# Kernel tuning notes

Measured on AMD Instinct MI355X. Metric: run time of the kernel, lower is better.

Reference implementation:

```python
import jax, jax.numpy as jnp
from jax import lax
import numpy as np

NF, G, K = 64, 8, 3
B, H, W = 4, 128, 128
KK = K * K
CG = NF // G  # channels per deformable group


def setup_inputs() -> dict:
    key = jax.random.key(0)
    ks = jax.random.split(key, 8)
    f32 = jnp.float32
    s = 0.05  # small init so predicted offsets stay in a realistic range
    return {
        'nbr_fea_l': jax.random.normal(ks[0], (B, NF, H, W), f32),
        'ref_fea_l': jax.random.normal(ks[1], (B, NF, H, W), f32),
        'w_off1': jax.random.normal(ks[2], (NF, 2 * NF, K, K), f32) * s,
        'b_off1': jax.random.normal(ks[3], (NF,), f32) * s,
        'w_om': jax.random.normal(ks[4], (3 * G * KK, NF, K, K), f32) * s,
        'b_om': jax.random.normal(ks[5], (3 * G * KK,), f32) * s,
        'w_dcn': jax.random.normal(ks[6], (NF, NF, K, K), f32) * s,
        'b_dcn': jax.random.normal(ks[7], (NF,), f32) * s,
    }


def _conv3(x, w, b):
    # 3x3, stride 1, pad 1, NCHW/OIHW
    y = lax.conv_general_dilated(x, w, (1, 1), ((1, 1), (1, 1)))
    return y + b[None, :, None, None]


def _lrelu(x):
    return jnp.where(x >= 0, x, 0.1 * x)


def _gather_one(xf, idx):
    # xf: [CG, H*W], idx: [KK, H, W] -> [CG, KK, H, W]
    return jnp.take(xf, idx, axis=1)


_gather = jax.vmap(jax.vmap(_gather_one))  # over B, G


def _bilinear(x_flat, py, px):
    # x_flat: [B,G,CG,H*W]; py/px: [B,G,KK,H,W] sample coords
    y0f = jnp.floor(py)
    x0f = jnp.floor(px)
    wy = py - y0f
    wx = px - x0f
    y0 = y0f.astype(jnp.int32)
    x0 = x0f.astype(jnp.int32)
    out = jnp.zeros(x_flat.shape[:3] + py.shape[2:], x_flat.dtype)
    corners = [(0, 0, (1 - wy) * (1 - wx)), (0, 1, (1 - wy) * wx),
               (1, 0, wy * (1 - wx)), (1, 1, wy * wx)]
    for dy, dx, wgt in corners:
        yy = y0 + dy
        xx = x0 + dx
        valid = ((yy >= 0) & (yy < H) & (xx >= 0) & (xx < W)).astype(x_flat.dtype)
        idx = jnp.clip(yy, 0, H - 1) * W + jnp.clip(xx, 0, W - 1)
        g = _gather(x_flat, idx)  # [B,G,CG,KK,H,W]
        out = out + g * (wgt * valid)[:, :, None]
    return out


def _forward(nbr, ref, w_off1, b_off1, w_om, b_om, w_dcn, b_dcn):
    # offset feature branch
    off_feat = _lrelu(_conv3(jnp.concatenate([nbr, ref], axis=1), w_off1, b_off1))
    om = _conv3(off_feat, w_om, b_om)  # [B, 3*G*KK, H, W]
    o1, o2, m = jnp.split(om, 3, axis=1)
    off_y = o1.reshape(B, G, KK, H, W)
    off_x = o2.reshape(B, G, KK, H, W)
    mask = jax.nn.sigmoid(m).reshape(B, G, KK, H, W)
    # kernel tap displacements (pad=1, dilation=1, stride=1)
    dy = (jnp.repeat(jnp.arange(K), K) - 1).astype(nbr.dtype)  # [KK]
    dx = (jnp.tile(jnp.arange(K), K) - 1).astype(nbr.dtype)
    hh = jnp.arange(H, dtype=nbr.dtype)
    ww = jnp.arange(W, dtype=nbr.dtype)
    py = hh[None, None, None, :, None] + dy[None, None, :, None, None] + off_y
    px = ww[None, None, None, None, :] + dx[None, None, :, None, None] + off_x
    x_flat = nbr.reshape(B, G, CG, H * W)
    sampled = _bilinear(x_flat, py, px)           # [B,G,CG,KK,H,W]
    sampled = sampled * mask[:, :, None]          # modulated (DCNv2)
    w = w_dcn.reshape(NF, G, CG, KK)
    out = jnp.einsum('bgckhw,ogck->bohw', sampled, w) + b_dcn[None, :, None, None]
    return _lrelu(out)


def reference(nbr_fea_l, ref_fea_l, w_off1, b_off1, w_om, b_om, w_dcn, b_dcn):
    return _forward(nbr_fea_l, ref_fea_l, w_off1, b_off1, w_om, b_om, w_dcn, b_dcn)
```

## Files before the change

kernel.cpp:

```cpp
#include <hip/hip_runtime.h>
#include <hip/hip_bf16.h>
#include <hip/hip_fp16.h>
#include <cmath>

#define NF 64
#define GRP 8
#define CG 8
#define KK 9
#define HH 128
#define WWID 128
#define BB 4
#define HWSZ (HH * WWID)
#define C_OM 216
#define OMS 292
#define DPS 72

typedef __attribute__((ext_vector_type(8))) short bf16x8;
typedef __attribute__((ext_vector_type(8))) _Float16 f16x8;
typedef __attribute__((ext_vector_type(4))) float f32x4;

__device__ inline unsigned short f2bf(float f) {
    union { float f; unsigned u; } x; x.f = f;
    unsigned r = x.u + 0x7fff + ((x.u >> 16) & 1);
    return (unsigned short)(r >> 16);
}

__global__ __launch_bounds__(256) void prep_kernel(
    const float* __restrict__ nbr, const float* __restrict__ ref,
    const float* __restrict__ w1, const float* __restrict__ wom,
    const float* __restrict__ wdcn,
    unsigned short* __restrict__ out, unsigned short* __restrict__ gm,
    unsigned short* __restrict__ wf1, unsigned short* __restrict__ wf2,
    unsigned short* __restrict__ wdf)
{
    __shared__ unsigned short lds[64 * 136];
    __shared__ __half lds_h[64 * 72];
    const int tid = threadIdx.x;

    if (blockIdx.x < 1024) {
        const int blk = blockIdx.x;
        const int b = blk >> 8, rem = blk & 255, y = rem >> 1, x0 = (rem & 1) * 64;
        const size_t rowoff = (size_t)y * WWID + x0;

        for (int it = 0; it < 32; ++it) {
            int idx = it * 256 + tid;
            int c = idx >> 6, p = idx & 63;
            const float* src = (c < NF) ? (nbr + (size_t)(b * NF + c) * HWSZ)
                                        : (ref + (size_t)(b * NF + c - NF) * HWSZ);
            const float v = src[rowoff + p];
            lds[p * 136 + c] = f2bf(v);
            if (c < 64) lds_h[p * 72 + c] = __float2half(v);
        }
        __syncthreads();
        const int p = tid >> 2, c0 = (tid & 3) * 32;
        unsigned short* dst = out + ((size_t)b * HWSZ + rowoff + p) * 128 + c0;
#pragma unroll
        for (int i = 0; i < 8; ++i)
            *(int2*)(dst + i * 4) = *(const int2*)&lds[p * 136 + c0 + i * 4];
        if (c0 < 64) {
#pragma unroll
            for (int gi = 0; gi < 4; ++gi) {
                const int g = (c0 >> 3) + gi;
                *(int4*)(gm + (((size_t)(b * 8 + g)) * HWSZ + rowoff + p) * 8) =
                    *(const int4*)&lds_h[p * 72 + g * 8];
            }
        }
        return;
    }

    int idx = (blockIdx.x - 1024) * 256 + tid;
    if (idx < 73728) {
        int j = idx & 7, lane = (idx >> 3) & 63, t = idx >> 9;
        int mt = t % 4, kt = t / 4;
        int c0 = (kt / 9) * 32, tap = kt - (kt / 9) * 9;
        int cout = mt * 16 + (lane & 15);
        int cin = c0 + ((lane >> 4) * 8) + j;
        wf1[idx] = f2bf(w1[((size_t)cout * 128 + cin) * KK + tap]);
        return;
    }
    idx -= 73728;
    if (idx < 129024) {
        int j = idx & 7, lane = (idx >> 3) & 63, t = idx >> 9;
        int mt = t % 14, kt = t / 14;
        int c0 = (kt / 9) * 32, tap = kt - (kt / 9) * 9;
        int cout = mt * 16 + (lane & 15);
        int cin = c0 + ((lane >> 4) * 8) + j;
        float v = (cout < C_OM) ? wom[((size_t)cout * 64 + cin) * KK + tap] : 0.f;
        wf2[idx] = f2bf(v);
        return;
    }
    idx -= 129024;
    if (idx < 36864) {
        int j = idx & 7, lane = (idx >> 3) & 63, t = idx >> 9;
        int mt = t & 3, s = t >> 2;
        int cout = mt * 16 + (lane & 15);
        int kglob = s * 32 + (lane >> 4) * 8 + j;
        int gk = kglob >> 3, c = kglob & 7;
        int g = gk / 9, kt = gk - g * 9;
        const __half hv = __float2half(wdcn[((size_t)cout * NF + g * 8 + c) * 9 + kt]);
        wdf[idx] = *(const unsigned short*)&hv;
    }
}

__global__ __launch_bounds__(256) void conv1_kernel(
    const unsigned short* __restrict__ in,
    const unsigned short* __restrict__ wf,
    const float* __restrict__ bias,
    unsigned short* __restrict__ dst)
{
    __shared__ unsigned short st[3 * 66 * DPS];

    const int tid = threadIdx.x;
    const int lane = tid & 63;
    const int wv = tid >> 6;
    const int ng = blockIdx.x;
    const int b = ng >> 8, rem = ng & 255;
    const int y = rem >> 1, x0 = (rem & 1) * 64;
    const int ln = lane & 15, kb = lane >> 4;

    f32x4 acc[4];
#pragma unroll
    for (int nt = 0; nt < 4; ++nt) acc[nt] = f32x4{0.f, 0.f, 0.f, 0.f};

    for (int ch0 = 0; ch0 < 128; ch0 += 64) {
        __syncthreads();
        for (int i = tid; i < 3 * 66 * 8; i += 256) {
            const int j = i & 7, t = i >> 3;
            const int px = t % 66, r = t / 66;
            const int yy = y + r - 1, xx = x0 + px - 1;
            int4 v = {0, 0, 0, 0};
            if ((unsigned)yy < (unsigned)HH && (unsigned)xx < (unsigned)WWID)
                v = *(const int4*)(in + ((size_t)b * HWSZ + yy * WWID + xx) * 128
                                      + ch0 + j * 8);
            *(int4*)&st[(r * 66 + px) * DPS + j * 8] = v;
        }
        __syncthreads();

#pragma unroll
        for (int cc = 0; cc < 64; cc += 32) {
#pragma unroll
            for (int tap = 0; tap < 9; ++tap) {
                const int ky = tap / 3, kx = tap % 3;
                const int kt = ((ch0 + cc) / 32) * 9 + tap;
                const bf16x8 afrag =
                    *(const bf16x8*)(wf + (((size_t)kt * 4 + wv) * 64 + lane) * 8);
                bf16x8 bfrag[4];
#pragma unroll
                for (int nt = 0; nt < 4; ++nt) {
                    const int px = nt * 16 + ln + kx;
                    bfrag[nt] = *(const bf16x8*)&st[(ky * 66 + px) * DPS + cc + kb * 8];
                }
#pragma unroll
                for (int nt = 0; nt < 4; ++nt)
                    acc[nt] = __builtin_amdgcn_mfma_f32_16x16x32_bf16(
                        afrag, bfrag[nt], acc[nt], 0, 0, 0);
            }
        }
    }

    const int cout = wv * 16 + kb * 4;
    const float b0 = bias[cout], b1 = bias[cout + 1];
    const float b2 = bias[cout + 2], b3 = bias[cout + 3];
#pragma unroll
    for (int nt = 0; nt < 4; ++nt) {
        const int px = x0 + nt * 16 + ln;
        const size_t pix = (size_t)b * HWSZ + (size_t)y * WWID + px;
        f32x4 v = acc[nt];
        v[0] += b0; v[1] += b1; v[2] += b2; v[3] += b3;
#pragma unroll
        for (int r = 0; r < 4; ++r) v[r] = (v[r] >= 0.f) ? v[r] : 0.1f * v[r];
        int2 pk;
        pk.x = (int)f2bf(v[0]) | ((int)f2bf(v[1]) << 16);
        pk.y = (int)f2bf(v[2]) | ((int)f2bf(v[3]) << 16);
        *(int2*)(dst + pix * 64 + cout) = pk;
    }
}

__global__ __launch_bounds__(256, 4) void dcn_fused_kernel(
    const unsigned short* __restrict__ off_f,
    const unsigned short* __restrict__ gm,
    const unsigned short* __restrict__ wf2,
    const float* __restrict__ bom,
    const unsigned short* __restrict__ wdf,
    const float* __restrict__ bdcn,
    float* __restrict__ out)
{
    __shared__ unsigned short smem[64 * OMS];

    const int raw = blockIdx.x;
    const int bid = (raw & 7) * 128 + (raw >> 3);
    const int b = bid >> 8;
    const int rem = bid & 255;
    const int y = rem >> 1;
    const int x0 = (rem & 1) * 64;

    const int tid = threadIdx.x;
    const int lane = tid & 63;
    const int wv = tid >> 6;
    const int ln = lane & 15, kb = lane >> 4;

    for (int i = tid; i < 3 * 66 * 8; i += 256) {
        const int j = i & 7, t = i >> 3;
        const int px = t % 66, r = t / 66;
        const int yy = y + r - 1, xx = x0 + px - 1;
        int4 v = {0, 0, 0, 0};
        if ((unsigned)yy < (unsigned)HH && (unsigned)xx < (unsigned)WWID)
            v = *(const int4*)(off_f + ((size_t)b * HWSZ + yy * WWID + xx) * 64 + j * 8);
        *(int4*)&smem[(r * 66 + px) * DPS + j * 8] = v;
    }
    __syncthreads();

    f32x4 acc1[4][4];
#pragma unroll
    for (int i = 0; i < 4; ++i)
#pragma unroll
        for (int j = 0; j < 4; ++j) acc1[i][j] = f32x4{0.f, 0.f, 0.f, 0.f};

    {
        bf16x8 afA[4], afB[4];
#pragma unroll
        for (int i = 0; i < 4; ++i) {
            const int mt = wv + 4 * i;
            afA[i] = (mt < 14)
                ? ((const bf16x8*)wf2)[(size_t)0 * 14 * 64 + (size_t)mt * 64 + lane]
                : bf16x8{};
        }

#pragma unroll
        for (int step = 0; step < 18; ++step) {
            const int cc = (step / 9) * 32;
            const int tap = step % 9;
            const int ky = tap / 3, kx = tap % 3;

            if (step < 17) {
                const int kt1 = step + 1;
                bf16x8* alt = (step & 1) ? afA : afB;
#pragma unroll
                for (int i = 0; i < 4; ++i) {
                    const int mt = wv + 4 * i;
                    alt[i] = (mt < 14)
                        ? ((const bf16x8*)wf2)[(size_t)kt1 * 14 * 64 + (size_t)mt * 64 + lane]
                        : bf16x8{};
                }
            }

            bf16x8 bfrag[4];
#pragma unroll
            for (int nt = 0; nt < 4; ++nt) {
                const int px = nt * 16 + ln + kx;
                bfrag[nt] = *(const bf16x8*)&smem[(ky * 66 + px) * DPS + cc + kb * 8];
            }

            const bf16x8* cur = (step & 1) ? afB : afA;
#pragma unroll
            for (int i = 0; i < 4; ++i) {
                const int mt = wv + 4 * i;
                if (mt < 14) {
#pragma unroll
                    for (int nt = 0; nt < 4; ++nt)
                        acc1[i][nt] = __builtin_amdgcn_mfma_f32_16x16x32_bf16(
                            cur[i], bfrag[nt], acc1[i][nt], 0, 0, 0);
                }
            }
        }
    }
    __syncthreads();

    __half* smh = (__half*)smem;
#pragma unroll
    for (int i = 0; i < 4; ++i) {
        const int mt = wv + 4 * i;
        if (mt >= 14) continue;
        const int cb = mt * 16 + kb * 4;
#pragma unroll
        for (int nt = 0; nt < 4; ++nt) {
            const int px = nt * 16 + ln;
#pragma unroll
            for (int r = 0; r < 4; ++r) {
                const int c = cb + r;
                if (c < C_OM) {
                    const int field = (c >= 144) ? 2 : ((c >= 72) ? 1 : 0);
                    const int gk = c - field * 72;
                    float v = acc1[i][nt][r] + bom[c];
                    if (field == 2) v = 1.f / (1.f + __expf(-v));
                    smh[px * OMS + gk * 4 + field] = __float2half(v);
                }
            }
        }
    }
    __syncthreads();

    const int pxl = wv * 16 + ln;
    const int x = x0 + pxl;

    f32x4 acc[4];
#pragma unroll
    for (int mt = 0; mt < 4; ++mt) acc[mt] = f32x4{0.f, 0.f, 0.f, 0.f};

    const unsigned short* gmb = gm + (size_t)b * 8 * HWSZ * 8;

#pragma unroll
    for (int ch = 0; ch < 3; ++ch) {
        short4 q[6];
#pragma unroll
        for (int i = 0; i < 6; ++i) {
            const int gk = (ch * 6 + i) * 4 + kb;
            q[i] = *(const short4*)&smh[pxl * OMS + gk * 4];
        }

#pragma unroll
        for (int i = 0; i < 6; ++i) {
            const int s = ch * 6 + i;
            const int gk = s * 4 + kb;
            const int g = gk / 9;
            const int kt = gk - g * 9;

            const float oy = __half2float(((const __half*)&q[i])[0]);
            const float ox = __half2float(((const __half*)&q[i])[1]);
            const float mv = __half2float(((const __half*)&q[i])[2]);

            const float pyf = (float)(y + kt / 3 - 1) + oy;
            const float pxf = (float)(x + kt % 3 - 1) + ox;
            const float fy = floorf(pyf), fx = floorf(pxf);
            const float wy = pyf - fy, wx = pxf - fx;
            const int iy = (int)fy, ix = (int)fx;

            float w00 = (1.f - wy) * (1.f - wx);
            float w01 = (1.f - wy) * wx;
            float w10 = wy * (1.f - wx);
            float w11 = wy * wx;

            const bool vy0 = (iy >= 0) && (iy < HH);
            const bool vy1 = (iy + 1 >= 0) && (iy + 1 < HH);
            const bool vx0 = (ix >= 0) && (ix < WWID);
            const bool vx1 = (ix + 1 >= 0) && (ix + 1 < WWID);
            w00 *= (vy0 && vx0) ? mv : 0.f;
            w01 *= (vy0 && vx1) ? mv : 0.f;
            w10 *= (vy1 && vx0) ? mv : 0.f;
            w11 *= (vy1 && vx1) ? mv : 0.f;

            const int y0c = min(max(iy, 0), HH - 1);
            const int y1c = min(max(iy + 1, 0), HH - 1);
            const int x0c = min(max(ix, 0), WWID - 1);
            const int x1c = min(max(ix + 1, 0), WWID - 1);
            const int sel = x1c - x0c;

            const float wl0 = w00 + (sel ? 0.f : w01);
            const float wh0 = sel ? w01 : 0.f;
            const float wl1 = w10 + (sel ? 0.f : w11);
            const float wh1 = sel ? w11 : 0.f;

            const unsigned short* pgm = gmb + (size_t)g * HWSZ * 8;
            const size_t rec0 = (size_t)(y0c * WWID + x0c) * 8;
            const size_t rec1 = (size_t)(y1c * WWID + x0c) * 8;
            int4 L0 = *(const int4*)(pgm + rec0);
            int4 H0 = *(const int4*)(pgm + rec0 + 8);
            int4 L1 = *(const int4*)(pgm + rec1);
            int4 H1 = *(const int4*)(pgm + rec1 + 8);

            const __half2 wl0h = __float2half2_rn(wl0);
            const __half2 wh0h = __float2half2_rn(wh0);
            const __half2 wl1h = __float2half2_rn(wl1);
            const __half2 wh1h = __float2half2_rn(wh1);
            const __half2* l0 = (const __half2*)&L0;
            const __half2* h0 = (const __half2*)&H0;
            const __half2* l1 = (const __half2*)&L1;
            const __half2* h1 = (const __half2*)&H1;
            __half2 bp0 = __hfma2(l0[0], wl0h, __hfma2(h0[0], wh0h,
                          __hfma2(l1[0], wl1h, __hmul2(h1[0], wh1h))));
            __half2 bp1 = __hfma2(l0[1], wl0h, __hfma2(h0[1], wh0h,
                          __hfma2(l1[1], wl1h, __hmul2(h1[1], wh1h))));
            __half2 bp2 = __hfma2(l0[2], wl0h, __hfma2(h0[2], wh0h,
                          __hfma2(l1[2], wl1h, __hmul2(h1[2], wh1h))));
            __half2 bp3 = __hfma2(l0[3], wl0h, __hfma2(h0[3], wh0h,
                          __hfma2(l1[3], wl1h, __hmul2(h1[3], wh1h))));
            __half2 bpv[4] = {bp0, bp1, bp2, bp3};
            const f16x8 bfrag = *(const f16x8*)bpv;

            const f16x8* af = (const f16x8*)wdf + ((size_t)s * 4) * 64 + lane;
#pragma unroll
            for (int mt = 0; mt < 4; ++mt)
                acc[mt] = __builtin_amdgcn_mfma_f32_16x16x32_f16(
                    af[(size_t)mt * 64], bfrag, acc[mt], 0, 0, 0);
        }
    }

#pragma unroll
    for (int mt = 0; mt < 4; ++mt) {
#pragma unroll
        for (int r = 0; r < 4; ++r) {
            const int cout = mt * 16 + kb * 4 + r;
            float v = acc[mt][r] + bdcn[cout];
            v = (v >= 0.f) ? v : 0.1f * v;
            out[((size_t)(b * NF + cout)) * HWSZ + (size_t)y * WWID + x] = v;
        }
    }
}

extern "C" void kernel_launch(void* const* d_in, const int* in_sizes, int n_in,
                              void* d_out, int out_size, void* d_ws, size_t ws_size,
                              hipStream_t stream)
{
    const float* nbr  = (const float*)d_in[0];
    const float* ref  = (const float*)d_in[1];
    const float* w1   = (const float*)d_in[2];
    const float* b1   = (const float*)d_in[3];
    const float* wom  = (const float*)d_in[4];
    const float* bom  = (const float*)d_in[5];
    const float* wdcn = (const float*)d_in[6];
    const float* bdcn = (const float*)d_in[7];
    float* out = (float*)d_out;

    const size_t NH_B  = (size_t)BB * HWSZ * 128 * 2;
    const size_t OFF_B = (size_t)BB * HWSZ * 64 * 2;
    const size_t GM_B  = (size_t)BB * HWSZ * 64 * 2 + 64;
    const size_t WF1_B = 36 * 4 * 512 * 2;
    const size_t WF2_B = 18 * 14 * 512 * 2;

    char* ws = (char*)d_ws;
    unsigned short* nhwcin = (unsigned short*)ws;
    unsigned short* off_f  = (unsigned short*)(ws + NH_B);
    unsigned short* gm     = (unsigned short*)(ws + NH_B + OFF_B);
    unsigned short* wf1    = (unsigned short*)(ws + NH_B + OFF_B + GM_B);
    unsigned short* wf2    = wf1 + WF1_B / 2;
    unsigned short* wdf    = wf2 + WF2_B / 2;

    prep_kernel<<<1024 + 936, 256, 0, stream>>>(
        nbr, ref, w1, wom, wdcn, nhwcin, gm, wf1, wf2, wdf);

    conv1_kernel<<<1024, 256, 0, stream>>>(nhwcin, wf1, b1, off_f);

    dcn_fused_kernel<<<1024, 256, 0, stream>>>(
        off_f, gm, wf2, bom, wdf, bdcn, out);
}
```

Before: 90.01 us.

## Widen DCN tile to full row, vectorize prep loads, double-buffer conv1 weights

The fused DCN kernel now handles a full 128-pixel row per 512-thread block, so the halo of the offset features is loaded once per row and each wave covers 8 pixel tiles with 2 channel tiles. The prep kernel reads inputs as float4 rather than scalars, and conv1 prefetches the next weight fragment while issuing MFMAs on the current one. The larger block doubles LDS use and changes occupancy and register pressure, and the launch-bounds hint of 4 blocks of 512 threads may be unreachable.

Result: no change. 88.38 us (median of 2 runs) (-1.8%).

```diff
diff --git a/kernel.cpp b/kernel.cpp
--- a/kernel.cpp
+++ b/kernel.cpp
@@ -42,14 +42,20 @@
         const int b = blk >> 8, rem = blk & 255, y = rem >> 1, x0 = (rem & 1) * 64;
         const size_t rowoff = (size_t)y * WWID + x0;
 
-        for (int it = 0; it < 32; ++it) {
+#pragma unroll
+        for (int it = 0; it < 8; ++it) {
             int idx = it * 256 + tid;
-            int c = idx >> 6, p = idx & 63;
+            int c = idx >> 4, p4 = idx & 15;
             const float* src = (c < NF) ? (nbr + (size_t)(b * NF + c) * HWSZ)
                                         : (ref + (size_t)(b * NF + c - NF) * HWSZ);
-            const float v = src[rowoff + p];
-            lds[p * 136 + c] = f2bf(v);
-            if (c < 64) lds_h[p * 72 + c] = __float2half(v);
+            const float4 v = *(const float4*)(src + rowoff + p4 * 4);
+            const float vv[4] = {v.x, v.y, v.z, v.w};
+#pragma unroll
+            for (int k = 0; k < 4; ++k) {
+                const int p = p4 * 4 + k;
+                lds[p * 136 + c] = f2bf(vv[k]);
+                if (c < 64) lds_h[p * 72 + c] = __float2half(vv[k]);
+            }
         }
         __syncthreads();
         const int p = tid >> 2, c0 = (tid & 3) * 32;
@@ -136,25 +142,34 @@
         }
         __syncthreads();
 
-#pragma unroll
-        for (int cc = 0; cc < 64; cc += 32) {
-#pragma unroll
-            for (int tap = 0; tap < 9; ++tap) {
-                const int ky = tap / 3, kx = tap % 3;
-                const int kt = ((ch0 + cc) / 32) * 9 + tap;
-                const bf16x8 afrag =
-                    *(const bf16x8*)(wf + (((size_t)kt * 4 + wv) * 64 + lane) * 8);
-                bf16x8 bfrag[4];
-#pragma unroll
-                for (int nt = 0; nt < 4; ++nt) {
-                    const int px = nt * 16 + ln + kx;
-                    bfrag[nt] = *(const bf16x8*)&st[(ky * 66 + px) * DPS + cc + kb * 8];
-                }
-#pragma unroll
-                for (int nt = 0; nt < 4; ++nt)
-                    acc[nt] = __builtin_amdgcn_mfma_f32_16x16x32_bf16(
-                        afrag, bfrag[nt], acc[nt], 0, 0, 0);
-            }
+        const int base_kt = (ch0 / 32) * 9;
+        bf16x8 afA, afB;
+        afA = *(const bf16x8*)(wf + (((size_t)base_kt * 4 + wv) * 64 + lane) * 8);
+
+#pragma unroll
+        for (int step = 0; step < 18; ++step) {
+            const int cc = (step / 9) * 32;
+            const int tap = step % 9;
+            const int ky = tap / 3, kx = tap % 3;
+
+            if (step < 17) {
+                const int kt1 = base_kt + step + 1;
+                bf16x8* alt = (step & 1) ? &afA : &afB;
+                *alt = *(const bf16x8*)(wf + (((size_t)kt1 * 4 + wv) * 64 + lane) * 8);
+            }
+
+            bf16x8 bfrag[4];
+#pragma unroll
+            for (int nt = 0; nt < 4; ++nt) {
+                const int px = nt * 16 + ln + kx;
+                bfrag[nt] = *(const bf16x8*)&st[(ky * 66 + px) * DPS + cc + kb * 8];
+            }
+
+            const bf16x8 cur = (step & 1) ? afB : afA;
+#pragma unroll
+            for (int nt = 0; nt < 4; ++nt)
+                acc[nt] = __builtin_amdgcn_mfma_f32_16x16x32_bf16(
+                    cur, bfrag[nt], acc[nt], 0, 0, 0);
         }
     }
 
@@ -176,7 +191,7 @@
     }
 }
 
-__global__ __launch_bounds__(256, 4) void dcn_fused_kernel(
+__global__ __launch_bounds__(512, 4) void dcn_fused_kernel(
     const unsigned short* __restrict__ off_f,
     const unsigned short* __restrict__ gm,
     const unsigned short* __restrict__ wf2,
@@ -185,44 +200,42 @@
     const float* __restrict__ bdcn,
     float* __restrict__ out)
 {
-    __shared__ unsigned short smem[64 * OMS];
+    __shared__ unsigned short smem[128 * OMS];
 
     const int raw = blockIdx.x;
-    const int bid = (raw & 7) * 128 + (raw >> 3);
-    const int b = bid >> 8;
-    const int rem = bid & 255;
-    const int y = rem >> 1;
-    const int x0 = (rem & 1) * 64;
+    const int bid = (raw & 7) * 64 + (raw >> 3);
+    const int b = bid >> 7;
+    const int y = bid & 127;
 
     const int tid = threadIdx.x;
     const int lane = tid & 63;
     const int wv = tid >> 6;
     const int ln = lane & 15, kb = lane >> 4;
 
-    for (int i = tid; i < 3 * 66 * 8; i += 256) {
+    for (int i = tid; i < 3 * 130 * 8; i += 512) {
         const int j = i & 7, t = i >> 3;
-        const int px = t % 66, r = t / 66;
-        const int yy = y + r - 1, xx = x0 + px - 1;
+        const int px = t % 130, r = t / 130;
+        const int yy = y + r - 1, xx = px - 1;
         int4 v = {0, 0, 0, 0};
         if ((unsigned)yy < (unsigned)HH && (unsigned)xx < (unsigned)WWID)
             v = *(const int4*)(off_f + ((size_t)b * HWSZ + yy * WWID + xx) * 64 + j * 8);
-        *(int4*)&smem[(r * 66 + px) * DPS + j * 8] = v;
+        *(int4*)&smem[(r * 130 + px) * DPS + j * 8] = v;
     }
     __syncthreads();
 
-    f32x4 acc1[4][4];
-#pragma unroll
-    for (int i = 0; i < 4; ++i)
-#pragma unroll
-        for (int j = 0; j < 4; ++j) acc1[i][j] = f32x4{0.f, 0.f, 0.f, 0.f};
+    f32x4 acc1[2][8];
+#pragma unroll
+    for (int i = 0; i < 2; ++i)
+#pragma unroll
+        for (int j = 0; j < 8; ++j) acc1[i][j] = f32x4{0.f, 0.f, 0.f, 0.f};
 
     {
-        bf16x8 afA[4], afB[4];
-#pragma unroll
-        for (int i = 0; i < 4; ++i) {
-            const int mt = wv + 4 * i;
+        bf16x8 afA[2], afB[2];
+#pragma unroll
+        for (int i = 0; i < 2; ++i) {
+            const int mt = wv + 8 * i;
             afA[i] = (mt < 14)
-                ? ((const bf16x8*)wf2)[(size_t)0 * 14 * 64 + (size_t)mt * 64 + lane]
+                ? ((const bf16x8*)wf2)[(size_t)mt * 64 + lane]
                 : bf16x8{};
         }
 
@@ -236,28 +249,28 @@
                 const int kt1 = step + 1;
                 bf16x8* alt = (step & 1) ? afA : afB;
 #pragma unroll
-                for (int i = 0; i < 4; ++i) {
-                    const int mt = wv + 4 * i;
+                for (int i = 0; i < 2; ++i) {
+                    const int mt = wv + 8 * i;
                     alt[i] = (mt < 14)
                         ? ((const bf16x8*)wf2)[(size_t)kt1 * 14 * 64 + (size_t)mt * 64 + lane]
                         : bf16x8{};
                 }
             }
 
-            bf16x8 bfrag[4];
-#pragma unroll
-            for (int nt = 0; nt < 4; ++nt) {
+            bf16x8 bfrag[8];
+#pragma unroll
+            for (int nt = 0; nt < 8; ++nt) {
                 const int px = nt * 16 + ln + kx;
-                bfrag[nt] = *(const bf16x8*)&smem[(ky * 66 + px) * DPS + cc + kb * 8];
+                bfrag[nt] = *(const bf16x8*)&smem[(ky * 130 + px) * DPS + cc + kb * 8];
             }
 
             const bf16x8* cur = (step & 1) ? afB : afA;
 #pragma unroll
-            for (int i = 0; i < 4; ++i) {
-                const int mt = wv + 4 * i;
+            for (int i = 0; i < 2; ++i) {
+                const int mt = wv + 8 * i;
                 if (mt < 14) {
 #pragma unroll
-                    for (int nt = 0; nt < 4; ++nt)
+                    for (int nt = 0; nt < 8; ++nt)
                         acc1[i][nt] = __builtin_amdgcn_mfma_f32_16x16x32_bf16(
                             cur[i], bfrag[nt], acc1[i][nt], 0, 0, 0);
                 }
@@ -268,12 +281,12 @@
 
     __half* smh = (__half*)smem;
 #pragma unroll
-    for (int i = 0; i < 4; ++i) {
-        const int mt = wv + 4 * i;
+    for (int i = 0; i < 2; ++i) {
+        const int mt = wv + 8 * i;
         if (mt >= 14) continue;
         const int cb = mt * 16 + kb * 4;
 #pragma unroll
-        for (int nt = 0; nt < 4; ++nt) {
+        for (int nt = 0; nt < 8; ++nt) {
             const int px = nt * 16 + ln;
 #pragma unroll
             for (int r = 0; r < 4; ++r) {
@@ -291,7 +304,7 @@
     __syncthreads();
 
     const int pxl = wv * 16 + ln;
-    const int x = x0 + pxl;
+    const int x = pxl;
 
     f32x4 acc[4];
 #pragma unroll
@@ -430,6 +443,6 @@
 
     conv1_kernel<<<1024, 256, 0, stream>>>(nhwcin, wf1, b1, off_f);
 
-    dcn_fused_kernel<<<1024, 256, 0, stream>>>(
+    dcn_fused_kernel<<<512, 512, 0, stream>>>(
         off_f, gm, wf2, bom, wdf, bdcn, out);
 }
```
